# Performance work log

Hardware: AMD Instinct MI355X
Metric: run time of the kernel (lower is better)

Reference implementation:

```python
import jax, jax.numpy as jnp
import numpy as np

B, S, E, D, A = 32, 2048, 1024, 1024, 1024


def setup_inputs() -> dict:
    key = jax.random.key(0)
    k1, k2, k3, k4, k5, k6, k7, k8 = jax.random.split(key, 8)
    # Kaiming-uniform-ish init scales (values don't matter for correctness)
    def lin(kw, kb, fan_in, fan_out):
        bound = 1.0 / np.sqrt(fan_in)
        W = jax.random.uniform(kw, (fan_out, fan_in), minval=-bound, maxval=bound, dtype=jnp.float32)
        b = jax.random.uniform(kb, (fan_out,), minval=-bound, maxval=bound, dtype=jnp.float32)
        return W, b
    W_enc, b_enc = lin(k1, k2, E, A)
    W_dec, b_dec = lin(k3, k4, D, A)
    W_v, b_v = lin(k5, k6, A, 1)
    encoder_out = jax.random.normal(k7, (B, S, E), dtype=jnp.float32)
    decoder_hidden = jax.random.normal(k8, (B, D), dtype=jnp.float32)
    return {
        "encoder_out": encoder_out,
        "decoder_hidden": decoder_hidden,
        "W_enc": W_enc, "b_enc": b_enc,
        "W_dec": W_dec, "b_dec": b_dec,
        "W_v": W_v, "b_v": b_v,
    }


def reference(encoder_out, decoder_hidden, W_enc, b_enc, W_dec, b_dec, W_v, b_v):
    # encoder_proj: [B, S, A]
    encoder_proj = jnp.einsum('bse,ae->bsa', encoder_out, W_enc) + b_enc
    # decoder_proj: [B, 1, A]
    decoder_proj = (jnp.einsum('bd,ad->ba', decoder_hidden, W_dec) + b_dec)[:, None, :]
    # scores: [B, S] (V projects attention_dim -> 1)
    scores = jnp.einsum('bsa,a->bs', jnp.tanh(encoder_proj + decoder_proj), W_v[0]) + b_v[0]
    alpha = jax.nn.softmax(scores, axis=1)  # [B, S]
    context = jnp.einsum('bse,bs->be', encoder_out, alpha)  # [B, E]
    return (context, alpha)
```

## Files before the change

kernel.cpp:

```cpp
#include <hip/hip_runtime.h>

typedef unsigned short ushort_t;
typedef __attribute__((ext_vector_type(8))) short short8;
typedef __attribute__((ext_vector_type(4))) float f32x4;


__device__ __forceinline__ ushort_t f2bf(float f) {
    unsigned u = __builtin_bit_cast(unsigned, f);
    u += 0x7fffu + ((u >> 16) & 1u);
    return (ushort_t)(u >> 16);
}

__device__ __forceinline__ float tanh_fast(float x) {
    float e = __expf(2.0f * x);
    float r = __builtin_amdgcn_rcpf(e + 1.0f);
    return __builtin_fmaf(-2.0f, r, 1.0f);
}

__device__ __forceinline__ void gld16(const ushort_t* g, ushort_t* lds) {
    __builtin_amdgcn_global_load_lds(
        (const __attribute__((address_space(1))) unsigned int*)g,
        (__attribute__((address_space(3))) unsigned int*)lds, 16, 0, 0);
}


__global__ __launch_bounds__(256) void k_prep(const float* __restrict__ enc,
                                              const float* __restrict__ Wenc,
                                              ushort_t* __restrict__ encB,
                                              ushort_t* __restrict__ wencB,
                                              float4* __restrict__ scores4) {
    int i = blockIdx.x * 256 + threadIdx.x;
    const int stride = gridDim.x * 256;
    for (; i < 17055744; i += stride) {
        if (i < 16777216) {
            float4 v = ((const float4*)enc)[i];
            ushort4 o;
            o.x = f2bf(v.x); o.y = f2bf(v.y); o.z = f2bf(v.z); o.w = f2bf(v.w);
            ((ushort4*)encB)[i] = o;
        } else if (i < 17039360) {
            int j = i - 16777216;
            float4 v = ((const float4*)Wenc)[j];
            ushort4 o;
            o.x = f2bf(v.x); o.y = f2bf(v.y); o.z = f2bf(v.z); o.w = f2bf(v.w);
            ((ushort4*)wencB)[j] = o;
        } else {
            scores4[i - 17039360] = (float4){0.f, 0.f, 0.f, 0.f};
        }
    }
}


__global__ __launch_bounds__(256) void k_dproj(const float* __restrict__ dh,
                                               const float* __restrict__ Wd,
                                               const float* __restrict__ bd,
                                               const float* __restrict__ be,
                                               float* __restrict__ dproj) {
    int wid = blockIdx.x * 4 + (threadIdx.x >> 6);
    int lane = threadIdx.x & 63;
    int a = wid & 1023, b = wid >> 10;
    const float4* x = (const float4*)(dh + (size_t)b * 1024);
    const float4* wrow = (const float4*)(Wd + (size_t)a * 1024);
    float s = 0.f;
#pragma unroll
    for (int it = 0; it < 4; ++it) {
        int c = it * 64 + lane;
        float4 xv = x[c], wv = wrow[c];
        s += xv.x * wv.x + xv.y * wv.y + xv.z * wv.z + xv.w * wv.w;
    }
#pragma unroll
    for (int o = 1; o < 64; o <<= 1) s += __shfl_xor(s, o, 64);
    if (lane == 0) dproj[b * 1024 + a] = s + bd[a] + be[a];
}


__global__ __launch_bounds__(256) void k_gemm_scores(const ushort_t* __restrict__ A,
                                                     const ushort_t* __restrict__ Bm,
                                                     const float* __restrict__ dproj,
                                                     const float* __restrict__ Wv,
                                                     float* __restrict__ scores) {
    __shared__ __align__(16) ushort_t At[128 * 64];
    __shared__ __align__(16) ushort_t Bt[128 * 64];

    const int tid = threadIdx.x;
    const int lane = tid & 63;
    const int w = tid >> 6;
    const int wm = w >> 1, wn = w & 1;

    const int blk = blockIdx.x;
    const int q2 = blk >> 3;
    const int blkN = q2 & 7;
    const int blkM = (blk & 7) + ((q2 >> 3) << 3);
    const long long arow0 = (long long)blkM * 128;
    const int brow0 = blkN * 128;

    const int sr = lane >> 3;
    const int sgrp = lane & 7;
    const int c8s = sgrp ^ sr;

    const int q = lane >> 4;
    const int ml = lane & 15;

    const ushort_t* ga = A + (arow0 + w * 32 + sr) * 1024 + c8s * 8;
    const ushort_t* gb = Bm + (long long)(brow0 + w * 32 + sr) * 1024 + c8s * 8;

    f32x4 acc[4][4];
#pragma unroll
    for (int i = 0; i < 4; ++i)
#pragma unroll
        for (int jj = 0; jj < 4; ++jj) acc[i][jj] = (f32x4){0.f, 0.f, 0.f, 0.f};

    for (int k0 = 0; k0 < 1024; k0 += 64) {
        __syncthreads();
#pragma unroll
        for (int j = 0; j < 4; ++j) {
            gld16(ga + j * 8192, &At[(w * 4 + j) * 512]);
            gld16(gb + j * 8192, &Bt[(w * 4 + j) * 512]);
        }
        ga += 64; gb += 64;
        __builtin_amdgcn_s_waitcnt(0);
        __syncthreads();

#pragma unroll
        for (int kk = 0; kk < 2; ++kk) {
            const int kb = kk * 4;
            short8 af[4], bfr[4];
#pragma unroll
            for (int i = 0; i < 4; ++i) {
                int row = wm * 64 + i * 16 + ml;
                int slot = (kb + q) ^ (row & 7);
                af[i] = *(const short8*)&At[row * 64 + slot * 8];
                int col = wn * 64 + i * 16 + ml;
                int slotb = (kb + q) ^ (col & 7);
                bfr[i] = *(const short8*)&Bt[col * 64 + slotb * 8];
            }
#pragma unroll
            for (int i = 0; i < 4; ++i)
#pragma unroll
                for (int jj = 0; jj < 4; ++jj)
                    acc[i][jj] = __builtin_amdgcn_mfma_f32_16x16x32_bf16(
                        af[i], bfr[jj], acc[i][jj], 0, 0, 0);
        }
    }

    const int bb = blkM >> 4;
#pragma unroll
    for (int i = 0; i < 4; ++i) {
        float rs[4] = {0.f, 0.f, 0.f, 0.f};
#pragma unroll
        for (int jj = 0; jj < 4; ++jj) {
            int a = blkN * 128 + wn * 64 + jj * 16 + ml;
            float dp = dproj[bb * 1024 + a];
            float wv = Wv[a];
            f32x4 v = acc[i][jj];
            rs[0] += wv * tanh_fast(v.x + dp);
            rs[1] += wv * tanh_fast(v.y + dp);
            rs[2] += wv * tanh_fast(v.z + dp);
            rs[3] += wv * tanh_fast(v.w + dp);
        }
#pragma unroll
        for (int r = 0; r < 4; ++r)
#pragma unroll
            for (int o = 1; o < 16; o <<= 1) rs[r] += __shfl_xor(rs[r], o, 64);
        if (ml == 0) {
            long long m0 = arow0 + wm * 64 + i * 16 + q * 4;
            atomicAdd(&scores[m0 + 0], rs[0]);
            atomicAdd(&scores[m0 + 1], rs[1]);
            atomicAdd(&scores[m0 + 2], rs[2]);
            atomicAdd(&scores[m0 + 3], rs[3]);
        }
    }
}


__global__ __launch_bounds__(256) void k_softmax(const float* __restrict__ scores,
                                                 float* __restrict__ out) {
    const int b = blockIdx.x, t = threadIdx.x;
    const int lane = t & 63, w = t >> 6;
    __shared__ float red[4];
    float v[8];
#pragma unroll
    for (int j = 0; j < 8; ++j) v[j] = scores[b * 2048 + j * 256 + t];
    float mx = v[0];
#pragma unroll
    for (int j = 1; j < 8; ++j) mx = fmaxf(mx, v[j]);
#pragma unroll
    for (int o = 1; o < 64; o <<= 1) mx = fmaxf(mx, __shfl_xor(mx, o, 64));
    if (lane == 0) red[w] = mx;
    __syncthreads();
    mx = fmaxf(fmaxf(red[0], red[1]), fmaxf(red[2], red[3]));
    float s = 0.f;
#pragma unroll
    for (int j = 0; j < 8; ++j) { v[j] = __expf(v[j] - mx); s += v[j]; }
#pragma unroll
    for (int o = 1; o < 64; o <<= 1) s += __shfl_xor(s, o, 64);
    __syncthreads();
    if (lane == 0) red[w] = s;
    __syncthreads();
    s = red[0] + red[1] + red[2] + red[3];
    float inv = 1.0f / s;
#pragma unroll
    for (int j = 0; j < 8; ++j) out[32768 + b * 2048 + j * 256 + t] = v[j] * inv;
}


__global__ __launch_bounds__(256) void k_context(const float* __restrict__ enc,
                                                 const float* __restrict__ alpha,
                                                 float* __restrict__ out) {
    const int b = blockIdx.x, ec = blockIdx.y, t = threadIdx.x;
    const int l = t & 31, g = t >> 5;
    __shared__ float al[2048];
    __shared__ f32x4 part[8][33];
#pragma unroll
    for (int j = 0; j < 8; ++j) al[j * 256 + t] = alpha[b * 2048 + j * 256 + t];
    __syncthreads();
    const float4* ep = (const float4*)enc + (size_t)b * 2048 * 256 + ec * 32 + l;
    const float* ag = &al[g * 256];
    f32x4 acc = (f32x4){0.f, 0.f, 0.f, 0.f};
#pragma unroll 8
    for (int s = 0; s < 256; ++s) {
        float4 ev = ep[(size_t)(g * 256 + s) * 256];
        float a = ag[s];
        acc.x += a * ev.x; acc.y += a * ev.y; acc.z += a * ev.z; acc.w += a * ev.w;
    }
    part[g][l] = acc;
    __syncthreads();
    if (t < 32) {
        f32x4 s = part[0][t];
#pragma unroll
        for (int gg = 1; gg < 8; ++gg) {
            f32x4 p = part[gg][t];
            s.x += p.x; s.y += p.y; s.z += p.z; s.w += p.w;
        }
        float4 o; o.x = s.x; o.y = s.y; o.z = s.z; o.w = s.w;
        ((float4*)(out + b * 1024 + ec * 128))[t] = o;
    }
}


extern "C" void kernel_launch(void* const* d_in, const int* in_sizes, int n_in,
                              void* d_out, int out_size, void* d_ws, size_t ws_size,
                              hipStream_t stream) {
    const float* enc  = (const float*)d_in[0];
    const float* dh   = (const float*)d_in[1];
    const float* Wenc = (const float*)d_in[2];
    const float* benc = (const float*)d_in[3];
    const float* Wdec = (const float*)d_in[4];
    const float* bdec = (const float*)d_in[5];
    const float* Wv   = (const float*)d_in[6];
    float* out = (float*)d_out;

    char* ws = (char*)d_ws;
    ushort_t* encB  = (ushort_t*)ws;
    ushort_t* wencB = (ushort_t*)(ws + 134217728ull);
    float* dproj    = (float*)(ws + 134217728ull + 2097152ull);
    float* scores   = (float*)(ws + 134217728ull + 2097152ull + 131072ull);

    k_prep<<<8192, 256, 0, stream>>>(enc, Wenc, encB, wencB, (float4*)scores);
    k_dproj<<<8192, 256, 0, stream>>>(dh, Wdec, bdec, benc, dproj);
    k_gemm_scores<<<4096, 256, 0, stream>>>(encB, wencB, dproj, Wv, scores);
    k_softmax<<<32, 256, 0, stream>>>(scores, out);
    k_context<<<dim3(32, 8), 256, 0, stream>>>(enc, out + 32768, out);
}
```

Baseline: 633.4 us.

## Double-buffer GEMM tiles, merge prep kernels, split context over sequence with bf16 reads

```diff
diff --git a/kernel.cpp b/kernel.cpp
--- a/kernel.cpp
+++ b/kernel.cpp
@@ -11,6 +11,11 @@
     return (ushort_t)(u >> 16);
 }
 
+__device__ __forceinline__ float bf2f(ushort_t h) {
+    unsigned u = ((unsigned)h) << 16;
+    return __builtin_bit_cast(float, u);
+}
+
 __device__ __forceinline__ float tanh_fast(float x) {
     float e = __expf(2.0f * x);
     float r = __builtin_amdgcn_rcpf(e + 1.0f);
@@ -23,63 +28,67 @@
         (__attribute__((address_space(3))) unsigned int*)lds, 16, 0, 0);
 }
 
-
-__global__ __launch_bounds__(256) void k_prep(const float* __restrict__ enc,
-                                              const float* __restrict__ Wenc,
-                                              ushort_t* __restrict__ encB,
-                                              ushort_t* __restrict__ wencB,
-                                              float4* __restrict__ scores4) {
-    int i = blockIdx.x * 256 + threadIdx.x;
-    const int stride = gridDim.x * 256;
-    for (; i < 17055744; i += stride) {
-        if (i < 16777216) {
-            float4 v = ((const float4*)enc)[i];
-            ushort4 o;
-            o.x = f2bf(v.x); o.y = f2bf(v.y); o.z = f2bf(v.z); o.w = f2bf(v.w);
-            ((ushort4*)encB)[i] = o;
-        } else if (i < 17039360) {
-            int j = i - 16777216;
-            float4 v = ((const float4*)Wenc)[j];
-            ushort4 o;
-            o.x = f2bf(v.x); o.y = f2bf(v.y); o.z = f2bf(v.z); o.w = f2bf(v.w);
-            ((ushort4*)wencB)[j] = o;
-        } else {
-            scores4[i - 17039360] = (float4){0.f, 0.f, 0.f, 0.f};
-        }
-    }
-}
-
-
-__global__ __launch_bounds__(256) void k_dproj(const float* __restrict__ dh,
+#define WAITCNT_VM8 (8 | (7 << 4) | (15 << 8))
+#define WAITCNT_VM0 (0 | (7 << 4) | (15 << 8))
+
+
+__global__ __launch_bounds__(256) void k_front(const float* __restrict__ enc,
+                                               const float* __restrict__ Wenc,
+                                               const float* __restrict__ dh,
                                                const float* __restrict__ Wd,
                                                const float* __restrict__ bd,
                                                const float* __restrict__ be,
-                                               float* __restrict__ dproj) {
-    int wid = blockIdx.x * 4 + (threadIdx.x >> 6);
-    int lane = threadIdx.x & 63;
-    int a = wid & 1023, b = wid >> 10;
-    const float4* x = (const float4*)(dh + (size_t)b * 1024);
-    const float4* wrow = (const float4*)(Wd + (size_t)a * 1024);
-    float s = 0.f;
-#pragma unroll
-    for (int it = 0; it < 4; ++it) {
-        int c = it * 64 + lane;
-        float4 xv = x[c], wv = wrow[c];
-        s += xv.x * wv.x + xv.y * wv.y + xv.z * wv.z + xv.w * wv.w;
-    }
-#pragma unroll
-    for (int o = 1; o < 64; o <<= 1) s += __shfl_xor(s, o, 64);
-    if (lane == 0) dproj[b * 1024 + a] = s + bd[a] + be[a];
-}
-
-
-__global__ __launch_bounds__(256) void k_gemm_scores(const ushort_t* __restrict__ A,
-                                                     const ushort_t* __restrict__ Bm,
-                                                     const float* __restrict__ dproj,
-                                                     const float* __restrict__ Wv,
-                                                     float* __restrict__ scores) {
-    __shared__ __align__(16) ushort_t At[128 * 64];
-    __shared__ __align__(16) ushort_t Bt[128 * 64];
+                                               ushort_t* __restrict__ encB,
+                                               ushort_t* __restrict__ wencB,
+                                               float* __restrict__ dproj,
+                                               float4* __restrict__ scores4) {
+    const int bx = blockIdx.x;
+    const int t = threadIdx.x;
+    if (bx < 8192) {
+        int i = bx * 256 + t;
+        for (; i < 17055744; i += 2097152) {
+            if (i < 16777216) {
+                float4 v = ((const float4*)enc)[i];
+                ushort4 o;
+                o.x = f2bf(v.x); o.y = f2bf(v.y); o.z = f2bf(v.z); o.w = f2bf(v.w);
+                ((ushort4*)encB)[i] = o;
+            } else if (i < 17039360) {
+                int j = i - 16777216;
+                float4 v = ((const float4*)Wenc)[j];
+                ushort4 o;
+                o.x = f2bf(v.x); o.y = f2bf(v.y); o.z = f2bf(v.z); o.w = f2bf(v.w);
+                ((ushort4*)wencB)[j] = o;
+            } else {
+                scores4[i - 17039360] = (float4){0.f, 0.f, 0.f, 0.f};
+            }
+        }
+    } else {
+        int wid = (bx - 8192) * 4 + (t >> 6);
+        int lane = t & 63;
+        int a = wid & 1023, b = wid >> 10;
+        const float4* x = (const float4*)(dh + (size_t)b * 1024);
+        const float4* wrow = (const float4*)(Wd + (size_t)a * 1024);
+        float s = 0.f;
+#pragma unroll
+        for (int it = 0; it < 4; ++it) {
+            int c = it * 64 + lane;
+            float4 xv = x[c], wv = wrow[c];
+            s += xv.x * wv.x + xv.y * wv.y + xv.z * wv.z + xv.w * wv.w;
+        }
+#pragma unroll
+        for (int o = 1; o < 64; o <<= 1) s += __shfl_xor(s, o, 64);
+        if (lane == 0) dproj[b * 1024 + a] = s + bd[a] + be[a];
+    }
+}
+
+
+__global__ __launch_bounds__(256, 2) void k_gemm_scores(const ushort_t* __restrict__ A,
+                                                        const ushort_t* __restrict__ Bm,
+                                                        const float* __restrict__ dproj,
+                                                        const float* __restrict__ Wv,
+                                                        float* __restrict__ scores) {
+    __shared__ __align__(16) ushort_t At[2][8192];
+    __shared__ __align__(16) ushort_t Bt[2][8192];
 
     const int tid = threadIdx.x;
     const int lane = tid & 63;
@@ -109,16 +118,29 @@
 #pragma unroll
         for (int jj = 0; jj < 4; ++jj) acc[i][jj] = (f32x4){0.f, 0.f, 0.f, 0.f};
 
-    for (int k0 = 0; k0 < 1024; k0 += 64) {
-        __syncthreads();
-#pragma unroll
-        for (int j = 0; j < 4; ++j) {
-            gld16(ga + j * 8192, &At[(w * 4 + j) * 512]);
-            gld16(gb + j * 8192, &Bt[(w * 4 + j) * 512]);
-        }
-        ga += 64; gb += 64;
-        __builtin_amdgcn_s_waitcnt(0);
-        __syncthreads();
+#pragma unroll
+    for (int j = 0; j < 4; ++j) {
+        gld16(ga + j * 8192, &At[0][(w * 4 + j) * 512]);
+        gld16(gb + j * 8192, &Bt[0][(w * 4 + j) * 512]);
+    }
+
+    for (int it = 0; it < 16; ++it) {
+        const int cur = it & 1;
+        if (it < 15) {
+            const ushort_t* ga2 = ga + (it + 1) * 64;
+            const ushort_t* gb2 = gb + (it + 1) * 64;
+#pragma unroll
+            for (int j = 0; j < 4; ++j) {
+                gld16(ga2 + j * 8192, &At[cur ^ 1][(w * 4 + j) * 512]);
+                gld16(gb2 + j * 8192, &Bt[cur ^ 1][(w * 4 + j) * 512]);
+            }
+            __builtin_amdgcn_s_waitcnt(WAITCNT_VM8);
+        } else {
+            __builtin_amdgcn_s_waitcnt(WAITCNT_VM0);
+        }
+        __atomic_signal_fence(__ATOMIC_ACQ_REL);
+        __builtin_amdgcn_s_barrier();
+        __atomic_signal_fence(__ATOMIC_ACQ_REL);
 
 #pragma unroll
         for (int kk = 0; kk < 2; ++kk) {
@@ -128,10 +150,10 @@
             for (int i = 0; i < 4; ++i) {
                 int row = wm * 64 + i * 16 + ml;
                 int slot = (kb + q) ^ (row & 7);
-                af[i] = *(const short8*)&At[row * 64 + slot * 8];
+                af[i] = *(const short8*)&At[cur][row * 64 + slot * 8];
                 int col = wn * 64 + i * 16 + ml;
                 int slotb = (kb + q) ^ (col & 7);
-                bfr[i] = *(const short8*)&Bt[col * 64 + slotb * 8];
+                bfr[i] = *(const short8*)&Bt[cur][col * 64 + slotb * 8];
             }
 #pragma unroll
             for (int i = 0; i < 4; ++i)
@@ -140,6 +162,9 @@
                     acc[i][jj] = __builtin_amdgcn_mfma_f32_16x16x32_bf16(
                         af[i], bfr[jj], acc[i][jj], 0, 0, 0);
         }
+        __atomic_signal_fence(__ATOMIC_ACQ_REL);
+        __builtin_amdgcn_s_barrier();
+        __atomic_signal_fence(__ATOMIC_ACQ_REL);
     }
 
     const int bb = blkM >> 4;
@@ -177,6 +202,8 @@
     const int b = blockIdx.x, t = threadIdx.x;
     const int lane = t & 63, w = t >> 6;
     __shared__ float red[4];
+#pragma unroll
+    for (int j = t; j < 1024; j += 256) out[b * 1024 + j] = 0.f;
     float v[8];
 #pragma unroll
     for (int j = 0; j < 8; ++j) v[j] = scores[b * 2048 + j * 256 + t];
@@ -203,24 +230,26 @@
 }
 
 
-__global__ __launch_bounds__(256) void k_context(const float* __restrict__ enc,
+__global__ __launch_bounds__(256) void k_context(const ushort_t* __restrict__ encB,
                                                  const float* __restrict__ alpha,
                                                  float* __restrict__ out) {
-    const int b = blockIdx.x, ec = blockIdx.y, t = threadIdx.x;
+    const int b = blockIdx.x, ec = blockIdx.y, sc = blockIdx.z, t = threadIdx.x;
     const int l = t & 31, g = t >> 5;
-    __shared__ float al[2048];
+    __shared__ float al[256];
     __shared__ f32x4 part[8][33];
-#pragma unroll
-    for (int j = 0; j < 8; ++j) al[j * 256 + t] = alpha[b * 2048 + j * 256 + t];
-    __syncthreads();
-    const float4* ep = (const float4*)enc + (size_t)b * 2048 * 256 + ec * 32 + l;
-    const float* ag = &al[g * 256];
+    al[t] = alpha[b * 2048 + sc * 256 + t];
+    __syncthreads();
+    const ushort_t* ep = encB + ((size_t)(b * 2048 + sc * 256 + g * 32)) * 1024 + ec * 128 + l * 4;
+    const float* ag = &al[g * 32];
     f32x4 acc = (f32x4){0.f, 0.f, 0.f, 0.f};
-#pragma unroll 8
-    for (int s = 0; s < 256; ++s) {
-        float4 ev = ep[(size_t)(g * 256 + s) * 256];
+#pragma unroll 4
+    for (int s = 0; s < 32; ++s) {
+        ushort4 ev = *(const ushort4*)(ep + (size_t)s * 1024);
         float a = ag[s];
-        acc.x += a * ev.x; acc.y += a * ev.y; acc.z += a * ev.z; acc.w += a * ev.w;
+        acc.x += a * bf2f(ev.x);
+        acc.y += a * bf2f(ev.y);
+        acc.z += a * bf2f(ev.z);
+        acc.w += a * bf2f(ev.w);
     }
     part[g][l] = acc;
     __syncthreads();
@@ -231,8 +260,11 @@
             f32x4 p = part[gg][t];
             s.x += p.x; s.y += p.y; s.z += p.z; s.w += p.w;
         }
-        float4 o; o.x = s.x; o.y = s.y; o.z = s.z; o.w = s.w;
-        ((float4*)(out + b * 1024 + ec * 128))[t] = o;
+        float* dst = out + b * 1024 + ec * 128 + t * 4;
+        atomicAdd(dst + 0, s.x);
+        atomicAdd(dst + 1, s.y);
+        atomicAdd(dst + 2, s.z);
+        atomicAdd(dst + 3, s.w);
     }
 }
 
@@ -255,9 +287,9 @@
     float* dproj    = (float*)(ws + 134217728ull + 2097152ull);
     float* scores   = (float*)(ws + 134217728ull + 2097152ull + 131072ull);
 
-    k_prep<<<8192, 256, 0, stream>>>(enc, Wenc, encB, wencB, (float4*)scores);
-    k_dproj<<<8192, 256, 0, stream>>>(dh, Wdec, bdec, benc, dproj);
+    k_front<<<16384, 256, 0, stream>>>(enc, Wenc, dh, Wdec, bdec, benc,
+                                       encB, wencB, dproj, (float4*)scores);
     k_gemm_scores<<<4096, 256, 0, stream>>>(encB, wencB, dproj, Wv, scores);
     k_softmax<<<32, 256, 0, stream>>>(scores, out);
-    k_context<<<dim3(32, 8), 256, 0, stream>>>(enc, out + 32768, out);
-}
+    k_context<<<dim3(32, 8, 8), 256, 0, stream>>>(encB, out + 32768, out);
+}
```

After: 598.6 us. 1.06x faster.
